# Optimization experiments

Measured on AMD Instinct MI355X. Metric: run time of the kernel, lower is better.

The kernel has to match this reference:

```python
import jax, jax.numpy as jnp
import numpy as np

EPS = 1e-5  # torch BatchNorm1d default eps


def setup_inputs() -> dict:
    key = jax.random.key(0)
    ks = jax.random.split(key, 12)
    B, D, H, R, T = 262144, 128, 64, 32, 8
    return {
        "x": jax.random.normal(ks[0], (B, D), dtype=jnp.float32),
        "t": jax.random.randint(ks[1], (B,), 0, T),
        # shared feature net: Linear(D->H), ReLU, BN(H) [eval mode], Dropout(eval=identity)
        "fw": jax.random.normal(ks[2], (H, D), dtype=jnp.float32) * 0.05,
        "fb": jax.random.normal(ks[3], (H,), dtype=jnp.float32) * 0.05,
        "f_gamma": jnp.ones((H,), jnp.float32),
        "f_beta": jnp.zeros((H,), jnp.float32),
        "f_mean": jax.random.normal(ks[4], (H,), dtype=jnp.float32) * 0.05,
        "f_var": jax.random.uniform(ks[5], (H,), minval=0.5, maxval=1.5),
        # T treatment heads, weights stacked on leading axis:
        # Linear(H->R), ReLU, BN(R), Dropout, Linear(R->1)
        "tw1": jax.random.normal(ks[6], (T, R, H), dtype=jnp.float32) * 0.05,
        "tb1": jax.random.normal(ks[7], (T, R), dtype=jnp.float32) * 0.05,
        "t_gamma": jnp.ones((T, R), jnp.float32),
        "t_beta": jnp.zeros((T, R), jnp.float32),
        "t_mean": jax.random.normal(ks[8], (T, R), dtype=jnp.float32) * 0.05,
        "t_var": jax.random.uniform(ks[9], (T, R), minval=0.5, maxval=1.5),
        "tw2": jax.random.normal(ks[10], (T, R), dtype=jnp.float32) * 0.05,  # [T,1,R] squeezed
        "tb2": jax.random.normal(ks[11], (T,), dtype=jnp.float32) * 0.05,
    }


def reference(x, t, fw, fb, f_gamma, f_beta, f_mean, f_var,
              tw1, tb1, t_gamma, t_beta, t_mean, t_var, tw2, tb2):
    # shared representation: Linear -> ReLU -> BN(eval) -> Dropout(identity)
    h = jax.nn.relu(x @ fw.T + fb)                                     # [B,H]
    h = f_gamma * (h - f_mean) * jax.lax.rsqrt(f_var + EPS) + f_beta   # [B,H]
    # run all T tiny heads densely, then select per-sample head (jit-friendly
    # equivalent of the boolean-mask gather/scatter loop; BN is eval-mode so
    # per-group masking and full-batch compute give identical math)
    z = jnp.einsum('bh,trh->btr', h, tw1) + tb1[None]                  # [B,T,R]
    z = jax.nn.relu(z)
    z = t_gamma[None] * (z - t_mean[None]) * jax.lax.rsqrt(t_var[None] + EPS) + t_beta[None]
    out_all = jnp.einsum('btr,tr->bt', z, tw2) + tb2[None]             # [B,T]
    pred = jnp.take_along_axis(out_all, t[:, None], axis=1)            # [B,1]
    return pred
```

## Files before the change

### kernel.cpp

```cpp
#include <hip/hip_runtime.h>
#include <hip/hip_bf16.h>
#include <cstdint>

#define EPS 1e-5f

typedef short bf16x8 __attribute__((ext_vector_type(8)));
typedef float f32x16 __attribute__((ext_vector_type(16)));
typedef unsigned int u32x4 __attribute__((ext_vector_type(4)));

#define WS_TW1S 0
#define WS_FWQ  8192
#define WS_FBQ  12800
#define WS_C2   12864
#define WS_TB1V 12880
#define WS_W2A  13056

static __device__ __forceinline__ unsigned short f2bf(float f) {
    unsigned int u = __float_as_uint(f);
    u += 0x7fffu + ((u >> 16) & 1u);
    return (unsigned short)(u >> 16);
}
static __device__ __forceinline__ short f2bf_fast(float f) {
    __hip_bfloat16 b = __float2bfloat16(f);
    return __builtin_bit_cast(short, b);
}
static __device__ __forceinline__ unsigned pk_bf16(float lo, float hi) {
    unsigned l = (unsigned)(unsigned short)__builtin_bit_cast(unsigned short, __float2bfloat16(lo));
    unsigned h = (unsigned)(unsigned short)__builtin_bit_cast(unsigned short, __float2bfloat16(hi));
    return l | (h << 16);
}

__global__ void tarnet_pre(
    const float* __restrict__ fw, const float* __restrict__ fb,
    const float* __restrict__ f_gamma, const float* __restrict__ f_beta,
    const float* __restrict__ f_mean,  const float* __restrict__ f_var,
    const float* __restrict__ tw1, const float* __restrict__ tb1,
    const float* __restrict__ t_gamma, const float* __restrict__ t_beta,
    const float* __restrict__ t_mean,  const float* __restrict__ t_var,
    const float* __restrict__ tw2, const float* __restrict__ tb2,
    float* __restrict__ ws)
{
    __shared__ float fs[64], fsh[64];
    const int i = threadIdx.x;
    if (i < 64) {
        float s = f_gamma[i] * rsqrtf(f_var[i] + EPS);
        fs[i]  = s;
        fsh[i] = f_beta[i] - f_mean[i] * s;
    }
    __syncthreads();

    unsigned short* tw1s_u = (unsigned short*)(ws + WS_TW1S);
    unsigned short* fwq_u  = (unsigned short*)(ws + WS_FWQ);
    unsigned short* tb1v_u = (unsigned short*)(ws + WS_TB1V);
    unsigned short* w2a_u  = (unsigned short*)(ws + WS_W2A);

    if (blockIdx.x == 0) {
        const int t = i >> 5, r = i & 31;
        const int idx = t * 32 + r;
        float tsc  = t_gamma[idx] * rsqrtf(t_var[idx] + EPS);
        float tb1s = tb1[idx];
        for (int j = 0; j < 64; ++j) {
            float w = tw1[idx * 64 + j];
            tb1s += w * fsh[j];
            int ht = j >> 5, qq = (j >> 3) & 3, h = (j >> 2) & 1, m = j & 3;
            int ks = ht * 2 + (qq >> 1);
            int ep = (qq & 1) * 4 + m;
            tw1s_u[(((t*4 + ks)*2 + h)*32 + r)*8 + ep] = f2bf(w * fs[j]);
        }
        tb1v_u[r*8 + t] = f2bf(tb1s);
        if (r == 0) {
            float a = tb2[t];
            for (int rr = 0; rr < 32; ++rr) {
                int id2 = t*32 + rr;
                float ts2 = t_gamma[id2] * rsqrtf(t_var[id2] + EPS);
                a += tw2[id2] * (t_beta[id2] - ts2 * t_mean[id2]);
            }
            ws[WS_C2 + t] = a;
        }
    } else {
        {
            const int hc = i >> 2, kq = (i & 3) * 32;
            for (int kk = 0; kk < 32; ++kk) {
                const int k = kq + kk;
                const int ks = k >> 4, h = (k >> 3) & 1, jj = k & 7;
                fwq_u[(((ks*2 + h)*64) + hc)*8 + jj] = f2bf(fw[hc*128 + k]);
            }
        }
        if (i < 64) {
            int ht = i >> 5, r32 = i & 31;
            int q  = ((r32 >> 3) << 2) | (r32 & 3);
            int hq = (r32 >> 2) & 1;
            ws[WS_FBQ + hq*32 + ht*16 + q] = fb[i];
        }
        {
            const int ln = i & 31, hh = (i >> 5) & 1, kt = (i >> 6) & 1, part = i >> 7;
            const int base = (((part*2 + kt)*2 + hh)*32 + ln)*8;
            for (int e = 0; e < 8; ++e) {
                unsigned short v = 0;
                if (ln < 8) {
                    const int rr = (e & 3) + 8*((e >> 2) & 1) + 16*kt + 4*hh;
                    const int id2 = ln*32 + rr;
                    float tsc = t_gamma[id2] * rsqrtf(t_var[id2] + EPS);
                    float w = tw2[id2] * tsc;
                    if (part == 0) v = f2bf(w);
                    else {
                        float whi = __uint_as_float(((unsigned)f2bf(w)) << 16);
                        v = f2bf(w - whi);
                    }
                }
                w2a_u[base + e] = v;
            }
        }
    }
}

__global__ __launch_bounds__(256, 3) void tarnet_main(
    const float* __restrict__ x, const int* __restrict__ t_arr,
    const float* __restrict__ ws, float* __restrict__ out)
{
    __shared__ unsigned short x_lds_u[128 * 128];
    char* xl = (char*)x_lds_u;

    const int tid  = threadIdx.x;
    const int wave = tid >> 6, lane = tid & 63;
    const int ln31 = lane & 31, hi = lane >> 5;
    const int sbase = blockIdx.x * 128;

    {
        const float4* xg = (const float4*)(x + (size_t)sbase * 128);
#pragma unroll
        for (int it = 0; it < 8; ++it) {
            const int i = it * 256 + tid;
            float4 a = xg[2*i], b = xg[2*i + 1];
            bf16x8 v;
            v[0] = f2bf_fast(a.x); v[1] = f2bf_fast(a.y);
            v[2] = f2bf_fast(a.z); v[3] = f2bf_fast(a.w);
            v[4] = f2bf_fast(b.x); v[5] = f2bf_fast(b.y);
            v[6] = f2bf_fast(b.z); v[7] = f2bf_fast(b.w);
            const int row = i >> 4, pcol = i & 15;
            *(bf16x8*)(xl + row * 256 + ((pcol * 16) ^ ((row & 15) << 4))) = v;
        }
    }
    __syncthreads();

    const unsigned short* fwq_u  = (const unsigned short*)(ws + WS_FWQ);
    const unsigned short* tw1s_u = (const unsigned short*)(ws + WS_TW1S);
    const unsigned short* w2a_u  = (const unsigned short*)(ws + WS_W2A);

    bf16x8 w2f[4];
#pragma unroll
    for (int pk = 0; pk < 4; ++pk)
        w2f[pk] = *(const bf16x8*)(w2a_u + ((pk*2 + hi)*32 + ln31)*8);
    const bf16x8 tb1v = *(const bf16x8*)((const unsigned short*)(ws + WS_TB1V) + ln31*8);
    u32x4 hbv = { hi ? 0u : 0x3F80u, 0u, 0u, 0u };
    const bf16x8 hbias = __builtin_bit_cast(bf16x8, hbv);

    const int tsel = t_arr[sbase + wave * 32 + ln31];
    const int srow = wave * 32 + ln31;
    const int rb = srow * 256, swz = (srow & 15) << 4;

    f32x16 acc[2];
    {
        const float* fbq = ws + WS_FBQ;
#pragma unroll
        for (int ht = 0; ht < 2; ++ht)
#pragma unroll
            for (int q = 0; q < 16; ++q)
                acc[ht][q] = fbq[hi*32 + ht*16 + q];
    }
#pragma unroll
    for (int ks = 0; ks < 8; ++ks) {
        bf16x8 wa0 = *(const bf16x8*)(fwq_u + (((ks*2 + hi)*64) + ln31     )*8);
        bf16x8 wa1 = *(const bf16x8*)(fwq_u + (((ks*2 + hi)*64) + ln31 + 32)*8);
        bf16x8 xf  = *(const bf16x8*)(xl + rb + ((ks*32 + hi*16) ^ swz));
        acc[0] = __builtin_amdgcn_mfma_f32_32x32x16_bf16(wa0, xf, acc[0], 0, 0, 0);
        acc[1] = __builtin_amdgcn_mfma_f32_32x32x16_bf16(wa1, xf, acc[1], 0, 0, 0);
    }

    bf16x8 hb[4];
    {
        unsigned w0[2][4], w1[2][4];
#pragma unroll
        for (int ht = 0; ht < 2; ++ht)
#pragma unroll
            for (int qq = 0; qq < 4; ++qq) {
                float a0 = fmaxf(acc[ht][qq*4+0], 0.f);
                float a1 = fmaxf(acc[ht][qq*4+1], 0.f);
                float a2 = fmaxf(acc[ht][qq*4+2], 0.f);
                float a3 = fmaxf(acc[ht][qq*4+3], 0.f);
                w0[ht][qq] = pk_bf16(a0, a1);
                w1[ht][qq] = pk_bf16(a2, a3);
            }
#pragma unroll
        for (int ks = 0; ks < 4; ++ks) {
            const int ht = ks >> 1, qa = (ks & 1) * 2;
            u32x4 wv = {w0[ht][qa], w1[ht][qa], w0[ht][qa+1], w1[ht][qa+1]};
            hb[ks] = __builtin_bit_cast(bf16x8, wv);
        }
    }

    float outv = 0.f;
#pragma unroll
    for (int tp = 0; tp < 4; ++tp) {
        const int ta = tp * 2, tb = tp * 2 + 1;
        f32x16 za = {0.f}, zc = {0.f};
#pragma unroll
        for (int ks = 0; ks < 4; ++ks) {
            bf16x8 awa = *(const bf16x8*)(tw1s_u + (((ta*4 + ks)*2 + hi)*32 + ln31)*8);
            bf16x8 awb = *(const bf16x8*)(tw1s_u + (((tb*4 + ks)*2 + hi)*32 + ln31)*8);
            za = __builtin_amdgcn_mfma_f32_32x32x16_bf16(awa, hb[ks], za, 0, 0, 0);
            zc = __builtin_amdgcn_mfma_f32_32x32x16_bf16(awb, hb[ks], zc, 0, 0, 0);
        }
        u32x4 tba = { hi ? 0u : (unsigned)(unsigned short)tb1v[ta], 0u, 0u, 0u };
        u32x4 tbb = { hi ? 0u : (unsigned)(unsigned short)tb1v[tb], 0u, 0u, 0u };
        za = __builtin_amdgcn_mfma_f32_32x32x16_bf16(
                 __builtin_bit_cast(bf16x8, tba), hbias, za, 0, 0, 0);
        zc = __builtin_amdgcn_mfma_f32_32x32x16_bf16(
                 __builtin_bit_cast(bf16x8, tbb), hbias, zc, 0, 0, 0);

        bf16x8 zba[2], zbb[2];
#pragma unroll
        for (int kt = 0; kt < 2; ++kt) {
            u32x4 wva, wvb;
#pragma unroll
            for (int wd = 0; wd < 4; ++wd) {
                wva[wd] = pk_bf16(fmaxf(za[8*kt + 2*wd], 0.f),
                                  fmaxf(za[8*kt + 2*wd + 1], 0.f));
                wvb[wd] = pk_bf16(fmaxf(zc[8*kt + 2*wd], 0.f),
                                  fmaxf(zc[8*kt + 2*wd + 1], 0.f));
            }
            zba[kt] = __builtin_bit_cast(bf16x8, wva);
            zbb[kt] = __builtin_bit_cast(bf16x8, wvb);
        }
        f32x16 da = {0.f}, db = {0.f};
        da = __builtin_amdgcn_mfma_f32_32x32x16_bf16(w2f[0], zba[0], da, 0, 0, 0);
        db = __builtin_amdgcn_mfma_f32_32x32x16_bf16(w2f[0], zbb[0], db, 0, 0, 0);
        da = __builtin_amdgcn_mfma_f32_32x32x16_bf16(w2f[1], zba[1], da, 0, 0, 0);
        db = __builtin_amdgcn_mfma_f32_32x32x16_bf16(w2f[1], zbb[1], db, 0, 0, 0);
        da = __builtin_amdgcn_mfma_f32_32x32x16_bf16(w2f[2], zba[0], da, 0, 0, 0);
        db = __builtin_amdgcn_mfma_f32_32x32x16_bf16(w2f[2], zbb[0], db, 0, 0, 0);
        da = __builtin_amdgcn_mfma_f32_32x32x16_bf16(w2f[3], zba[1], da, 0, 0, 0);
        db = __builtin_amdgcn_mfma_f32_32x32x16_bf16(w2f[3], zbb[1], db, 0, 0, 0);

        {
            float cand  = da[ta & 3];
            float other = __shfl_xor(cand, 32);
            float val   = (hi == (ta >> 2)) ? cand : other;
            outv = (ta == tsel) ? val : outv;
        }
        {
            float cand  = db[tb & 3];
            float other = __shfl_xor(cand, 32);
            float val   = (hi == (tb >> 2)) ? cand : other;
            outv = (tb == tsel) ? val : outv;
        }
    }
    outv += ws[WS_C2 + tsel];
    if (!hi) out[sbase + wave * 32 + ln31] = outv;
}

extern "C" void kernel_launch(void* const* d_in, const int* in_sizes, int n_in,
                              void* d_out, int out_size, void* d_ws, size_t ws_size,
                              hipStream_t stream) {
    const float* x       = (const float*)d_in[0];
    const int*   t       = (const int*)  d_in[1];
    const float* fw      = (const float*)d_in[2];
    const float* fb      = (const float*)d_in[3];
    const float* f_gamma = (const float*)d_in[4];
    const float* f_beta  = (const float*)d_in[5];
    const float* f_mean  = (const float*)d_in[6];
    const float* f_var   = (const float*)d_in[7];
    const float* tw1     = (const float*)d_in[8];
    const float* tb1     = (const float*)d_in[9];
    const float* t_gamma = (const float*)d_in[10];
    const float* t_beta  = (const float*)d_in[11];
    const float* t_mean  = (const float*)d_in[12];
    const float* t_var   = (const float*)d_in[13];
    const float* tw2     = (const float*)d_in[14];
    const float* tb2     = (const float*)d_in[15];

    float* ws   = (float*)d_ws;
    float* outp = (float*)d_out;
    const int B = in_sizes[0] / 128;

    tarnet_pre<<<2, 256, 0, stream>>>(fw, fb, f_gamma, f_beta, f_mean, f_var,
                                      tw1, tb1, t_gamma, t_beta, t_mean, t_var,
                                      tw2, tb2, ws);
    tarnet_main<<<B / 128, 256, 0, stream>>>(x, t, ws, outp);
}
```

Before: 51.92 us.

## Cut register pressure: bias via MFMA, single-head loop, four blocks per CU

The shared-layer bias is now applied with an extra MFMA against a bf16 bias fragment instead of preloading 32 fp32 accumulator values. The treatment-head loop handles one head per iteration instead of two, which halves the live accumulator tiles. Launch bounds rise from three to four blocks per CU to gain occupancy. The cost is less MFMA interleaving inside each wave, bf16 rounding of the first-layer bias, and possible spilling if registers no longer fit.

```diff
diff --git a/kernel.cpp b/kernel.cpp
--- a/kernel.cpp
+++ b/kernel.cpp
@@ -14,6 +14,7 @@
 #define WS_C2   12864
 #define WS_TB1V 12880
 #define WS_W2A  13056
+#define WS_FBA  14080
 
 static __device__ __forceinline__ unsigned short f2bf(float f) {
     unsigned int u = __float_as_uint(f);
@@ -53,6 +54,7 @@
     unsigned short* fwq_u  = (unsigned short*)(ws + WS_FWQ);
     unsigned short* tb1v_u = (unsigned short*)(ws + WS_TB1V);
     unsigned short* w2a_u  = (unsigned short*)(ws + WS_W2A);
+    unsigned short* fba_u  = (unsigned short*)(ws + WS_FBA);
 
     if (blockIdx.x == 0) {
         const int t = i >> 5, r = i & 31;
@@ -86,11 +88,13 @@
                 fwq_u[(((ks*2 + h)*64) + hc)*8 + jj] = f2bf(fw[hc*128 + k]);
             }
         }
-        if (i < 64) {
-            int ht = i >> 5, r32 = i & 31;
-            int q  = ((r32 >> 3) << 2) | (r32 & 3);
-            int hq = (r32 >> 2) & 1;
-            ws[WS_FBQ + hq*32 + ht*16 + q] = fb[i];
+        {
+            if (i < 128) {
+                const int r = i & 31, hh = (i >> 5) & 1, ht = (i >> 6) & 1;
+                const int base = ((ht*2 + hh)*32 + r)*8;
+                for (int e = 0; e < 8; ++e)
+                    fba_u[base + e] = (e == 0 && hh == 0) ? f2bf(fb[ht*32 + r]) : 0;
+            }
         }
         {
             const int ln = i & 31, hh = (i >> 5) & 1, kt = (i >> 6) & 1, part = i >> 7;
@@ -114,7 +118,7 @@
     }
 }
 
-__global__ __launch_bounds__(256, 3) void tarnet_main(
+__global__ __launch_bounds__(256, 4) void tarnet_main(
     const float* __restrict__ x, const int* __restrict__ t_arr,
     const float* __restrict__ ws, float* __restrict__ out)
 {
@@ -146,12 +150,17 @@
     const unsigned short* fwq_u  = (const unsigned short*)(ws + WS_FWQ);
     const unsigned short* tw1s_u = (const unsigned short*)(ws + WS_TW1S);
     const unsigned short* w2a_u  = (const unsigned short*)(ws + WS_W2A);
+    const unsigned short* fba_u  = (const unsigned short*)(ws + WS_FBA);
 
     bf16x8 w2f[4];
 #pragma unroll
     for (int pk = 0; pk < 4; ++pk)
         w2f[pk] = *(const bf16x8*)(w2a_u + ((pk*2 + hi)*32 + ln31)*8);
     const bf16x8 tb1v = *(const bf16x8*)((const unsigned short*)(ws + WS_TB1V) + ln31*8);
+    bf16x8 fba[2];
+#pragma unroll
+    for (int ht = 0; ht < 2; ++ht)
+        fba[ht] = *(const bf16x8*)(fba_u + ((ht*2 + hi)*32 + ln31)*8);
     u32x4 hbv = { hi ? 0u : 0x3F80u, 0u, 0u, 0u };
     const bf16x8 hbias = __builtin_bit_cast(bf16x8, hbv);
 
@@ -159,15 +168,7 @@
     const int srow = wave * 32 + ln31;
     const int rb = srow * 256, swz = (srow & 15) << 4;
 
-    f32x16 acc[2];
-    {
-        const float* fbq = ws + WS_FBQ;
-#pragma unroll
-        for (int ht = 0; ht < 2; ++ht)
-#pragma unroll
-            for (int q = 0; q < 16; ++q)
-                acc[ht][q] = fbq[hi*32 + ht*16 + q];
-    }
+    f32x16 acc[2] = {{0.f}, {0.f}};
 #pragma unroll
     for (int ks = 0; ks < 8; ++ks) {
         bf16x8 wa0 = *(const bf16x8*)(fwq_u + (((ks*2 + hi)*64) + ln31     )*8);
@@ -176,6 +177,8 @@
         acc[0] = __builtin_amdgcn_mfma_f32_32x32x16_bf16(wa0, xf, acc[0], 0, 0, 0);
         acc[1] = __builtin_amdgcn_mfma_f32_32x32x16_bf16(wa1, xf, acc[1], 0, 0, 0);
     }
+    acc[0] = __builtin_amdgcn_mfma_f32_32x32x16_bf16(fba[0], hbias, acc[0], 0, 0, 0);
+    acc[1] = __builtin_amdgcn_mfma_f32_32x32x16_bf16(fba[1], hbias, acc[1], 0, 0, 0);
 
     bf16x8 hb[4];
     {
@@ -201,59 +204,37 @@
 
     float outv = 0.f;
 #pragma unroll
-    for (int tp = 0; tp < 4; ++tp) {
-        const int ta = tp * 2, tb = tp * 2 + 1;
-        f32x16 za = {0.f}, zc = {0.f};
+    for (int th = 0; th < 8; ++th) {
+        f32x16 z = {0.f};
 #pragma unroll
         for (int ks = 0; ks < 4; ++ks) {
-            bf16x8 awa = *(const bf16x8*)(tw1s_u + (((ta*4 + ks)*2 + hi)*32 + ln31)*8);
-            bf16x8 awb = *(const bf16x8*)(tw1s_u + (((tb*4 + ks)*2 + hi)*32 + ln31)*8);
-            za = __builtin_amdgcn_mfma_f32_32x32x16_bf16(awa, hb[ks], za, 0, 0, 0);
-            zc = __builtin_amdgcn_mfma_f32_32x32x16_bf16(awb, hb[ks], zc, 0, 0, 0);
-        }
-        u32x4 tba = { hi ? 0u : (unsigned)(unsigned short)tb1v[ta], 0u, 0u, 0u };
-        u32x4 tbb = { hi ? 0u : (unsigned)(unsigned short)tb1v[tb], 0u, 0u, 0u };
-        za = __builtin_amdgcn_mfma_f32_32x32x16_bf16(
-                 __builtin_bit_cast(bf16x8, tba), hbias, za, 0, 0, 0);
-        zc = __builtin_amdgcn_mfma_f32_32x32x16_bf16(
-                 __builtin_bit_cast(bf16x8, tbb), hbias, zc, 0, 0, 0);
-
-        bf16x8 zba[2], zbb[2];
+            bf16x8 aw = *(const bf16x8*)(tw1s_u + (((th*4 + ks)*2 + hi)*32 + ln31)*8);
+            z = __builtin_amdgcn_mfma_f32_32x32x16_bf16(aw, hb[ks], z, 0, 0, 0);
+        }
+        u32x4 tbv = { hi ? 0u : (unsigned)(unsigned short)tb1v[th], 0u, 0u, 0u };
+        z = __builtin_amdgcn_mfma_f32_32x32x16_bf16(
+                __builtin_bit_cast(bf16x8, tbv), hbias, z, 0, 0, 0);
+
+        bf16x8 zb[2];
 #pragma unroll
         for (int kt = 0; kt < 2; ++kt) {
-            u32x4 wva, wvb;
-#pragma unroll
-            for (int wd = 0; wd < 4; ++wd) {
-                wva[wd] = pk_bf16(fmaxf(za[8*kt + 2*wd], 0.f),
-                                  fmaxf(za[8*kt + 2*wd + 1], 0.f));
-                wvb[wd] = pk_bf16(fmaxf(zc[8*kt + 2*wd], 0.f),
-                                  fmaxf(zc[8*kt + 2*wd + 1], 0.f));
-            }
-            zba[kt] = __builtin_bit_cast(bf16x8, wva);
-            zbb[kt] = __builtin_bit_cast(bf16x8, wvb);
-        }
-        f32x16 da = {0.f}, db = {0.f};
-        da = __builtin_amdgcn_mfma_f32_32x32x16_bf16(w2f[0], zba[0], da, 0, 0, 0);
-        db = __builtin_amdgcn_mfma_f32_32x32x16_bf16(w2f[0], zbb[0], db, 0, 0, 0);
-        da = __builtin_amdgcn_mfma_f32_32x32x16_bf16(w2f[1], zba[1], da, 0, 0, 0);
-        db = __builtin_amdgcn_mfma_f32_32x32x16_bf16(w2f[1], zbb[1], db, 0, 0, 0);
-        da = __builtin_amdgcn_mfma_f32_32x32x16_bf16(w2f[2], zba[0], da, 0, 0, 0);
-        db = __builtin_amdgcn_mfma_f32_32x32x16_bf16(w2f[2], zbb[0], db, 0, 0, 0);
-        da = __builtin_amdgcn_mfma_f32_32x32x16_bf16(w2f[3], zba[1], da, 0, 0, 0);
-        db = __builtin_amdgcn_mfma_f32_32x32x16_bf16(w2f[3], zbb[1], db, 0, 0, 0);
-
-        {
-            float cand  = da[ta & 3];
-            float other = __shfl_xor(cand, 32);
-            float val   = (hi == (ta >> 2)) ? cand : other;
-            outv = (ta == tsel) ? val : outv;
-        }
-        {
-            float cand  = db[tb & 3];
-            float other = __shfl_xor(cand, 32);
-            float val   = (hi == (tb >> 2)) ? cand : other;
-            outv = (tb == tsel) ? val : outv;
-        }
+            u32x4 wv;
+#pragma unroll
+            for (int wd = 0; wd < 4; ++wd)
+                wv[wd] = pk_bf16(fmaxf(z[8*kt + 2*wd], 0.f),
+                                 fmaxf(z[8*kt + 2*wd + 1], 0.f));
+            zb[kt] = __builtin_bit_cast(bf16x8, wv);
+        }
+        f32x16 d = {0.f};
+        d = __builtin_amdgcn_mfma_f32_32x32x16_bf16(w2f[0], zb[0], d, 0, 0, 0);
+        d = __builtin_amdgcn_mfma_f32_32x32x16_bf16(w2f[1], zb[1], d, 0, 0, 0);
+        d = __builtin_amdgcn_mfma_f32_32x32x16_bf16(w2f[2], zb[0], d, 0, 0, 0);
+        d = __builtin_amdgcn_mfma_f32_32x32x16_bf16(w2f[3], zb[1], d, 0, 0, 0);
+
+        float cand  = d[th & 3];
+        float other = __shfl_xor(cand, 32);
+        float val   = (hi == (th >> 2)) ? cand : other;
+        outv = (th == tsel) ? val : outv;
     }
     outv += ws[WS_C2 + tsel];
     if (!hi) out[sbase + wave * 32 + ln31] = outv;
```

Result: slower. 56.10 us (+8.0%).
